# Kernel optimization log

Hardware: AMD Instinct MI355X
Metric: run time of the kernel (lower is better)

Reference implementation:

```python
import jax, jax.numpy as jnp
import numpy as np

NUM_SCOPE = 64
NUM_SAMPLE = 16
DIM_ENCODE = 64


def _fixed_basis(dim):
    # FixedTimeEncoder / FixedFrequencyEncoder basis: w_i = 1 / 10^(9*i/(dim-1))
    return (1.0 / 10.0 ** jnp.linspace(0.0, 9.0, dim)).astype(jnp.float32)


def _cos_encode(t, dim):
    # t: [...] -> [..., dim]
    w = _fixed_basis(dim)
    return jnp.cos(t[..., None] * w)


def setup_inputs() -> dict:
    key = jax.random.key(0)
    ks = jax.random.split(key, 12)
    n, b, df = 4096, NUM_SCOPE, 172
    s_in = 1.0 / np.sqrt(df)
    return {
        "root_node_feature": jax.random.normal(ks[0], (n, df), jnp.float32),
        "root_ts": jax.random.uniform(ks[1], (n,), jnp.float32) * 1e4,
        "neighbor_node_feature": jax.random.normal(ks[2], (n, b, df), jnp.float32),
        "neighbor_edge_feature": jax.random.normal(ks[3], (n, b, df), jnp.float32),
        "neighbor_ts": jax.random.uniform(ks[4], (n, b), jnp.float32) * 1e4,
        "neighbor_nid": jax.random.randint(ks[5], (n, b), 0, 10000, jnp.int64) if jax.config.jax_enable_x64 else jax.random.randint(ks[5], (n, b), 0, 10000, jnp.int32),
        "W_node": jax.random.normal(ks[6], (df, 64), jnp.float32) * s_in,
        "b_node": jnp.zeros((64,), jnp.float32),
        "W_edge": jax.random.normal(ks[7], (df, 64), jnp.float32) * s_in,
        "b_edge": jnp.zeros((64,), jnp.float32),
        "W_link": jax.random.normal(ks[8], (320, 256), jnp.float32) / np.sqrt(320),
        "W_root": jax.random.normal(ks[9], (192, 256), jnp.float32) / np.sqrt(192),
    }


def reference(root_node_feature, root_ts, neighbor_node_feature,
              neighbor_edge_feature, neighbor_ts, neighbor_nid,
              W_node, b_node, W_edge, b_edge, W_link, W_root):
    n, b = neighbor_nid.shape
    # --- encode root node ---
    root_feat = jax.nn.relu(root_node_feature @ W_node + b_node)          # [n,64]
    root_time = _cos_encode(jnp.zeros((n,), jnp.float32), DIM_ENCODE)     # [n,64]
    root_freq = _cos_encode(jnp.ones((n,), jnp.float32), DIM_ENCODE)      # [n,64]
    root_encode = jnp.concatenate([root_feat, root_time, root_freq], 1)   # [n,192]
    # --- encode links ---
    node_enc = jax.nn.relu(neighbor_node_feature @ W_node + b_node)       # [n,b,64]
    edge_enc = jax.nn.relu(neighbor_edge_feature @ W_edge + b_edge)       # [n,b,64]
    neigh_time = root_ts[:, None] - neighbor_ts                           # [n,b]
    time_enc = _cos_encode(neigh_time, DIM_ENCODE)                        # [n,b,64]
    # pairwise equality mask + frequency count (keep_dummy_freq=True)
    neigh_mask = (neighbor_nid[:, :, None] == neighbor_nid[:, None, :])   # [n,b,b]
    neigh_freq = neigh_mask.sum(-1).astype(jnp.float32) / NUM_SCOPE       # [n,b]
    freq_enc = _cos_encode(neigh_freq, DIM_ENCODE)                        # [n,b,64]
    iden_enc = neigh_mask.astype(jnp.float32)                             # [n,b,b]
    link_encode = jnp.concatenate(
        [node_enc, edge_enc, time_enc, freq_enc, iden_enc], axis=-1)      # [n,b,320]
    # --- link mapper: project links & root, score, softmax over neighbors ---
    h_link = jax.nn.relu(jnp.einsum('nbd,dh->nbh', link_encode, W_link))  # [n,b,256]
    h_root = jax.nn.relu(root_encode @ W_root)                            # [n,256]
    scores = jnp.einsum('nbh,nh->nb', h_link, h_root) / jnp.sqrt(256.0)
    probs = jax.nn.softmax(scores, axis=-1)                               # [n,b]
    # --- weighted sampling WITHOUT replacement via Gumbel top-k ---
    g = jax.random.gumbel(jax.random.key(42), (n, b), jnp.float32)
    logp = jnp.log(probs + 1e-20)
    _, action = jax.lax.top_k(logp + g, NUM_SAMPLE)                       # [n,num_sample]
    return probs, action
```

## Files before the change

### kernel.cpp

```cpp
#include <hip/hip_runtime.h>
#include <cstdint>
#include <math.h>

#define B       64
#define DF      172
#define HDIM    256
#define KSAMP   16
#define THREADS 512

typedef const __attribute__((address_space(1))) unsigned int* gp_t;
typedef __attribute__((address_space(3))) unsigned int* lp_t;

#define FMA4(A_, S_, W_) \
  A_.x = fmaf(S_, W_.x, A_.x); A_.y = fmaf(S_, W_.y, A_.y); \
  A_.z = fmaf(S_, W_.z, A_.z); A_.w = fmaf(S_, W_.w, A_.w);

__device__ __forceinline__ uint32_t rotl32(uint32_t x, int d) {
  return (x << d) | (x >> (32 - d));
}

__device__ __forceinline__ void threefry2x32(uint32_t k0, uint32_t k1,
                                             uint32_t& x0, uint32_t& x1) {
  const uint32_t ks0 = k0, ks1 = k1, ks2 = k0 ^ k1 ^ 0x1BD11BDAu;
  x0 += ks0; x1 += ks1;
#define TF_R4(ra,rb,rc,rd) \
  x0 += x1; x1 = rotl32(x1, ra); x1 ^= x0; \
  x0 += x1; x1 = rotl32(x1, rb); x1 ^= x0; \
  x0 += x1; x1 = rotl32(x1, rc); x1 ^= x0; \
  x0 += x1; x1 = rotl32(x1, rd); x1 ^= x0;
  TF_R4(13,15,26,6)  x0 += ks1; x1 += ks2 + 1u;
  TF_R4(17,29,16,24) x0 += ks2; x1 += ks0 + 2u;
  TF_R4(13,15,26,6)  x0 += ks0; x1 += ks1 + 3u;
  TF_R4(17,29,16,24) x0 += ks1; x1 += ks2 + 4u;
  TF_R4(13,15,26,6)  x0 += ks2; x1 += ks0 + 5u;
#undef TF_R4
}

__device__ __forceinline__ void stage_async(const float* __restrict__ g,
                                            float* l, int t) {
#pragma unroll
  for (int it = 0; it < 5; ++it) {
    const int i  = it * 512 + t;
    const int ib = it * 512 + (t & ~63);
    __builtin_amdgcn_global_load_lds((gp_t)(g + i * 4), (lp_t)(l + ib * 4), 16, 0, 0);
  }
  if (t < 192) {
    const int i  = 2560 + t;
    const int ib = 2560 + (t & ~63);
    __builtin_amdgcn_global_load_lds((gp_t)(g + i * 4), (lp_t)(l + ib * 4), 16, 0, 0);
  }
}

__device__ __forceinline__ void enc_gemm(const float* __restrict__ stage,
                                         const float* __restrict__ W,
                                         const float* __restrict__ bias,
                                         float* __restrict__ out,
                                         int b2, int cg) {
  const float4* W4 = (const float4*)W;
  const float4* A0 = (const float4*)(stage + (2 * b2) * DF);
  const float4* A1 = (const float4*)(stage + (2 * b2 + 1) * DF);
  float4 acc0 = ((const float4*)bias)[cg];
  float4 acc1 = acc0;
  float4 w0 = W4[0 * 16 + cg], w1 = W4[1 * 16 + cg];
  float4 w2 = W4[2 * 16 + cg], w3 = W4[3 * 16 + cg];
  for (int k = 0; k < DF; k += 4) {
    const float4 wa = w0, wb = w1, wc = w2, wd = w3;
    if (k < DF - 4) {
      w0 = W4[(k + 4) * 16 + cg]; w1 = W4[(k + 5) * 16 + cg];
      w2 = W4[(k + 6) * 16 + cg]; w3 = W4[(k + 7) * 16 + cg];
    }
    const float4 x0 = A0[k >> 2];
    const float4 x1 = A1[k >> 2];
    FMA4(acc0, x0.x, wa) FMA4(acc0, x0.y, wb) FMA4(acc0, x0.z, wc) FMA4(acc0, x0.w, wd)
    FMA4(acc1, x1.x, wa) FMA4(acc1, x1.y, wb) FMA4(acc1, x1.z, wc) FMA4(acc1, x1.w, wd)
  }
  float4 o0 = make_float4(fmaxf(acc0.x, 0.f), fmaxf(acc0.y, 0.f), fmaxf(acc0.z, 0.f), fmaxf(acc0.w, 0.f));
  float4 o1 = make_float4(fmaxf(acc1.x, 0.f), fmaxf(acc1.y, 0.f), fmaxf(acc1.z, 0.f), fmaxf(acc1.w, 0.f));
  ((float4*)out)[(2 * b2) * 16 + cg]     = o0;
  ((float4*)out)[(2 * b2 + 1) * 16 + cg] = o1;
}

__device__ __forceinline__ void accum16(float2 (&acc)[16],
                                        const float* __restrict__ enc, int r16,
                                        const float2* __restrict__ Wlp) {
  float2 w0 = Wlp[0], w1 = Wlp[128], w2 = Wlp[256], w3 = Wlp[384];
  for (int d0 = 0; d0 < 64; d0 += 4) {
    const float2 wa = w0, wb = w1, wc = w2, wd = w3;
    if (d0 < 60) {
      const float2* p = Wlp + (d0 + 4) * 128;
      w0 = p[0]; w1 = p[128]; w2 = p[256]; w3 = p[384];
    }
#pragma unroll
    for (int i = 0; i < 16; ++i) {
      const float4 e = *(const float4*)&enc[(r16 + i) * 64 + d0];
      acc[i].x = fmaf(e.x, wa.x, acc[i].x); acc[i].y = fmaf(e.x, wa.y, acc[i].y);
      acc[i].x = fmaf(e.y, wb.x, acc[i].x); acc[i].y = fmaf(e.y, wb.y, acc[i].y);
      acc[i].x = fmaf(e.z, wc.x, acc[i].x); acc[i].y = fmaf(e.z, wc.y, acc[i].y);
      acc[i].x = fmaf(e.w, wd.x, acc[i].x); acc[i].y = fmaf(e.w, wd.y, acc[i].y);
    }
  }
}

__global__ __launch_bounds__(THREADS, 4)
void AdaptSampler_kernel(const float* __restrict__ rootf,
                         const float* __restrict__ root_ts,
                         const float* __restrict__ nf,
                         const float* __restrict__ ef,
                         const float* __restrict__ nts,
                         const int*   __restrict__ nid,
                         const float* __restrict__ Wn,
                         const float* __restrict__ bn,
                         const float* __restrict__ We,
                         const float* __restrict__ be,
                         const float* __restrict__ Wl,
                         const float* __restrict__ Wr,
                         float* __restrict__ out_probs,
                         float* __restrict__ out_action)
{
  __shared__ float nf_stage[B * DF];
  __shared__ float encA[B * 64];
  __shared__ float encB[B * 64];
  __shared__ float hroot_lds[HDIM];
  __shared__ float rootenc_lds[192];
  __shared__ float w_lds[B];
  __shared__ float ts_lds[B];
  __shared__ __align__(16) int nid_lds[B];
  __shared__ float freq_lds[B];
  __shared__ unsigned long long mask_lds[B];
  __shared__ float scpart[4][16][2];

  const int n = blockIdx.x;
  const int t = threadIdx.x;
  const int c2  = t & 127;
  const int r16 = (t >> 7) * 16;
  const int b2 = t >> 4;
  const int cg = t & 15;
  const float2* Wl2 = (const float2*)Wl;

  stage_async(nf + (size_t)n * B * DF, nf_stage, t);
  if (t >= 448) {
    const int j = t - 448;
    double e = 9.0 * (double)j / 63.0;
    const float wj = (float)(1.0 / pow(10.0, e));
    w_lds[j]   = wj;
    nid_lds[j] = nid[n * B + j];
    ts_lds[j]  = nts[n * B + j];
    float a = bn[j];
    const float* rr = rootf + (size_t)n * DF;
#pragma unroll 4
    for (int d = 0; d < DF; ++d) a = fmaf(rr[d], Wn[d * 64 + j], a);
    rootenc_lds[j]       = fmaxf(a, 0.0f);
    rootenc_lds[64 + j]  = 1.0f;
    rootenc_lds[128 + j] = cosf(wj);
  }
  __syncthreads();

  enc_gemm(nf_stage, Wn, bn, encA, b2, cg);
  {
    const float rts = root_ts[n];
#pragma unroll
    for (int q = 0; q < 8; ++q) {
      const int idx = q * 512 + t;
      const int bb = idx >> 6, dd = idx & 63;
      encB[idx] = cosf((rts - ts_lds[bb]) * w_lds[dd]);
    }
  }
  {
    const int h = t >> 1, hf = t & 1;
    float a = 0.0f;
    for (int d = hf * 96; d < hf * 96 + 96; ++d)
      a = fmaf(rootenc_lds[d], Wr[d * HDIM + h], a);
    a += __shfl_xor(a, 1);
    if (hf == 0) hroot_lds[h] = fmaxf(a, 0.0f);
  }
  if (t >= 448) {
    const int j = t - 448;
    const int my = nid_lds[j];
    unsigned long long m = 0ull;
    for (int k = 0; k < B; ++k)
      m |= ((unsigned long long)(nid_lds[k] == my)) << k;
    mask_lds[j] = m;
    freq_lds[j] = (float)__popcll(m) * 0.015625f;
  }
  __syncthreads();

  stage_async(ef + (size_t)n * B * DF, nf_stage, t);
  float2 acc[16];
#pragma unroll
  for (int i = 0; i < 16; ++i) acc[i] = make_float2(0.f, 0.f);
  accum16(acc, encA, r16, Wl2 + c2);
  __syncthreads();

  enc_gemm(nf_stage, We, be, encA, b2, cg);
  __syncthreads();

  accum16(acc, encA, r16, Wl2 + 64 * 128 + c2);
  __syncthreads();

#pragma unroll
  for (int q = 0; q < 8; ++q) {
    const int idx = q * 512 + t;
    const int bb = idx >> 6, dd = idx & 63;
    encA[idx] = cosf(freq_lds[bb] * w_lds[dd]);
  }
  __syncthreads();

  accum16(acc, encB, r16, Wl2 + 128 * 128 + c2);
  accum16(acc, encA, r16, Wl2 + 192 * 128 + c2);
  {
    const float2* Wlp = Wl2 + 256 * 128 + c2;
#pragma unroll
    for (int i = 0; i < 16; ++i) {
      unsigned long long m = mask_lds[r16 + i];
      while (m) {
        const int d = __builtin_ctzll(m);
        m &= m - 1;
        const float2 wv = Wlp[d * 128];
        acc[i].x += wv.x;
        acc[i].y += wv.y;
      }
    }
  }

  {
    const float2 hr = ((const float2*)hroot_lds)[c2];
#pragma unroll
    for (int i = 0; i < 16; ++i) {
      float s = fmaxf(acc[i].x, 0.f) * hr.x;
      s = fmaf(fmaxf(acc[i].y, 0.f), hr.y, s);
#pragma unroll
      for (int mm = 32; mm >= 1; mm >>= 1) s += __shfl_xor(s, mm);
      if ((t & 63) == 0) scpart[t >> 7][i][(t >> 6) & 1] = s;
    }
  }
  __syncthreads();

  if (t < B) {
    float s = (scpart[t >> 4][t & 15][0] + scpart[t >> 4][t & 15][1]) * 0.0625f;
    float m = s;
#pragma unroll
    for (int mm = 32; mm >= 1; mm >>= 1) m = fmaxf(m, __shfl_xor(m, mm));
    float e = expf(s - m);
    float sum = e;
#pragma unroll
    for (int mm = 32; mm >= 1; mm >>= 1) sum += __shfl_xor(sum, mm);
    float p = e / sum;
    out_probs[(size_t)n * B + t] = p;

    uint32_t i = (uint32_t)(n * B + t);
    uint32_t x0 = 0u, x1 = i;
    threefry2x32(0u, 42u, x0, x1);
    uint32_t bits = x0 ^ x1;
    float f = __uint_as_float((bits >> 9) | 0x3f800000u) - 1.0f;
    const float TINY = 1.1754943508222875e-38f;
    float u = fmaxf(f * (1.0f - TINY) + TINY, TINY);
    float g = -logf(-logf(u));
    float keyv = logf(p + 1e-20f) + g;

    float v = keyv;
    for (int k = 0; k < KSAMP; ++k) {
      float bv = v; int bi = t;
#pragma unroll
      for (int mm = 32; mm >= 1; mm >>= 1) {
        float ov = __shfl_xor(bv, mm);
        int   oi = __shfl_xor(bi, mm);
        if (ov > bv || (ov == bv && oi < bi)) { bv = ov; bi = oi; }
      }
      if (t == 0) out_action[(size_t)n * KSAMP + k] = (float)bi;
      if (t == bi) v = -3.402823466e+38f;
    }
  }
}

extern "C" void kernel_launch(void* const* d_in, const int* in_sizes, int n_in,
                              void* d_out, int out_size, void* d_ws, size_t ws_size,
                              hipStream_t stream) {
  const float* rootf = (const float*)d_in[0];
  const float* rts   = (const float*)d_in[1];
  const float* nf    = (const float*)d_in[2];
  const float* ef    = (const float*)d_in[3];
  const float* nts   = (const float*)d_in[4];
  const int*   nid   = (const int*)d_in[5];
  const float* Wn    = (const float*)d_in[6];
  const float* bn    = (const float*)d_in[7];
  const float* We    = (const float*)d_in[8];
  const float* be    = (const float*)d_in[9];
  const float* Wl    = (const float*)d_in[10];
  const float* Wr    = (const float*)d_in[11];

  const int n = in_sizes[1];
  float* probs  = (float*)d_out;
  float* action = probs + (size_t)n * B;

  AdaptSampler_kernel<<<dim3(n), dim3(THREADS), 0, stream>>>(
      rootf, rts, nf, ef, nts, nid, Wn, bn, We, be, Wl, Wr, probs, action);
}
```

Measured before the change: 882.4 us.

## Deepen weight prefetch in enc_gemm, move mask build earlier, drop one barrier

The encoder GEMM loop now keeps three groups of weight loads in flight with a manual 3-stage rotation instead of one-step lookahead. The neighbor-id mask and frequency computation moves into the first setup block. The frequency cosine encoding is written into the free staging buffer so it can overlap with the edge-encoding accumulation, removing one __syncthreads. This adds register pressure from the extra float4 prefetch registers and reuses the staging buffer, which has to be free by then.

```diff
diff --git a/kernel.cpp b/kernel.cpp
--- a/kernel.cpp
+++ b/kernel.cpp
@@ -51,6 +51,16 @@
   }
 }
 
+#define ENC_STEP(W0_, W1_, W2_, W3_, KK_) { \
+  const float4 x0 = A0[(KK_) >> 2]; \
+  const float4 x1 = A1[(KK_) >> 2]; \
+  FMA4(acc0, x0.x, W0_) FMA4(acc0, x0.y, W1_) FMA4(acc0, x0.z, W2_) FMA4(acc0, x0.w, W3_) \
+  FMA4(acc1, x1.x, W0_) FMA4(acc1, x1.y, W1_) FMA4(acc1, x1.z, W2_) FMA4(acc1, x1.w, W3_) }
+
+#define ENC_LOAD(W0_, W1_, W2_, W3_, KK_) { \
+  W0_ = W4[(KK_) * 16 + cg]; W1_ = W4[((KK_) + 1) * 16 + cg]; \
+  W2_ = W4[((KK_) + 2) * 16 + cg]; W3_ = W4[((KK_) + 3) * 16 + cg]; }
+
 __device__ __forceinline__ void enc_gemm(const float* __restrict__ stage,
                                          const float* __restrict__ W,
                                          const float* __restrict__ bias,
@@ -61,19 +71,19 @@
   const float4* A1 = (const float4*)(stage + (2 * b2 + 1) * DF);
   float4 acc0 = ((const float4*)bias)[cg];
   float4 acc1 = acc0;
-  float4 w0 = W4[0 * 16 + cg], w1 = W4[1 * 16 + cg];
-  float4 w2 = W4[2 * 16 + cg], w3 = W4[3 * 16 + cg];
-  for (int k = 0; k < DF; k += 4) {
-    const float4 wa = w0, wb = w1, wc = w2, wd = w3;
-    if (k < DF - 4) {
-      w0 = W4[(k + 4) * 16 + cg]; w1 = W4[(k + 5) * 16 + cg];
-      w2 = W4[(k + 6) * 16 + cg]; w3 = W4[(k + 7) * 16 + cg];
-    }
-    const float4 x0 = A0[k >> 2];
-    const float4 x1 = A1[k >> 2];
-    FMA4(acc0, x0.x, wa) FMA4(acc0, x0.y, wb) FMA4(acc0, x0.z, wc) FMA4(acc0, x0.w, wd)
-    FMA4(acc1, x1.x, wa) FMA4(acc1, x1.y, wb) FMA4(acc1, x1.z, wc) FMA4(acc1, x1.w, wd)
-  }
+  float4 a0, a1, a2, a3, b0, b1, b2_, b3, c0, c1, c2, c3;
+  ENC_LOAD(a0, a1, a2, a3, 0)
+  ENC_LOAD(b0, b1, b2_, b3, 4)
+  ENC_LOAD(c0, c1, c2, c3, 8)
+  for (int k0 = 0; k0 < 156; k0 += 12) {
+    ENC_STEP(a0, a1, a2, a3, k0)       ENC_LOAD(a0, a1, a2, a3, k0 + 12)
+    ENC_STEP(b0, b1, b2_, b3, k0 + 4)  ENC_LOAD(b0, b1, b2_, b3, k0 + 16)
+    ENC_STEP(c0, c1, c2, c3, k0 + 8)   ENC_LOAD(c0, c1, c2, c3, k0 + 20)
+  }
+  ENC_STEP(a0, a1, a2, a3, 156)  ENC_LOAD(a0, a1, a2, a3, 168)
+  ENC_STEP(b0, b1, b2_, b3, 160)
+  ENC_STEP(c0, c1, c2, c3, 164)
+  ENC_STEP(a0, a1, a2, a3, 168)
   float4 o0 = make_float4(fmaxf(acc0.x, 0.f), fmaxf(acc0.y, 0.f), fmaxf(acc0.z, 0.f), fmaxf(acc0.w, 0.f));
   float4 o1 = make_float4(fmaxf(acc1.x, 0.f), fmaxf(acc1.y, 0.f), fmaxf(acc1.z, 0.f), fmaxf(acc1.w, 0.f));
   ((float4*)out)[(2 * b2) * 16 + cg]     = o0;
@@ -152,6 +162,12 @@
     rootenc_lds[j]       = fmaxf(a, 0.0f);
     rootenc_lds[64 + j]  = 1.0f;
     rootenc_lds[128 + j] = cosf(wj);
+    const int my = nid_lds[j];
+    unsigned long long m = 0ull;
+    for (int k = 0; k < B; ++k)
+      m |= ((unsigned long long)(nid_lds[k] == my)) << k;
+    mask_lds[j] = m;
+    freq_lds[j] = (float)__popcll(m) * 0.015625f;
   }
   __syncthreads();
 
@@ -173,15 +189,6 @@
     a += __shfl_xor(a, 1);
     if (hf == 0) hroot_lds[h] = fmaxf(a, 0.0f);
   }
-  if (t >= 448) {
-    const int j = t - 448;
-    const int my = nid_lds[j];
-    unsigned long long m = 0ull;
-    for (int k = 0; k < B; ++k)
-      m |= ((unsigned long long)(nid_lds[k] == my)) << k;
-    mask_lds[j] = m;
-    freq_lds[j] = (float)__popcll(m) * 0.015625f;
-  }
   __syncthreads();
 
   stage_async(ef + (size_t)n * B * DF, nf_stage, t);
@@ -192,21 +199,19 @@
   __syncthreads();
 
   enc_gemm(nf_stage, We, be, encA, b2, cg);
-  __syncthreads();
-
-  accum16(acc, encA, r16, Wl2 + 64 * 128 + c2);
   __syncthreads();
 
 #pragma unroll
   for (int q = 0; q < 8; ++q) {
     const int idx = q * 512 + t;
     const int bb = idx >> 6, dd = idx & 63;
-    encA[idx] = cosf(freq_lds[bb] * w_lds[dd]);
-  }
+    nf_stage[idx] = cosf(freq_lds[bb] * w_lds[dd]);
+  }
+  accum16(acc, encA, r16, Wl2 + 64 * 128 + c2);
   __syncthreads();
 
   accum16(acc, encB, r16, Wl2 + 128 * 128 + c2);
-  accum16(acc, encA, r16, Wl2 + 192 * 128 + c2);
+  accum16(acc, nf_stage, r16, Wl2 + 192 * 128 + c2);
   {
     const float2* Wlp = Wl2 + 256 * 128 + c2;
 #pragma unroll
```

Result: slower. 966.2 us (+9.5%).

## Read encoder inputs directly from global and drop LDS staging buffer

Applied to the files above, without the earlier changes.

Removes the async global-to-LDS staging of neighbor node/edge features and has the encoder GEMM read rows straight from global memory with software prefetch. Both encoder GEMMs now run back to back into separate LDS buffers, the mask computation moves earlier, and several barriers disappear. The freed LDS and a higher launch-bounds occupancy hint aim to fit more blocks per CU. It risks uncoalesced strided global reads and register spilling under the tighter register budget.

```diff
diff --git a/kernel.cpp b/kernel.cpp
--- a/kernel.cpp
+++ b/kernel.cpp
@@ -7,9 +7,6 @@
 #define HDIM    256
 #define KSAMP   16
 #define THREADS 512
-
-typedef const __attribute__((address_space(1))) unsigned int* gp_t;
-typedef __attribute__((address_space(3))) unsigned int* lp_t;
 
 #define FMA4(A_, S_, W_) \
   A_.x = fmaf(S_, W_.x, A_.x); A_.y = fmaf(S_, W_.y, A_.y); \
@@ -36,43 +33,32 @@
 #undef TF_R4
 }
 
-__device__ __forceinline__ void stage_async(const float* __restrict__ g,
-                                            float* l, int t) {
-#pragma unroll
-  for (int it = 0; it < 5; ++it) {
-    const int i  = it * 512 + t;
-    const int ib = it * 512 + (t & ~63);
-    __builtin_amdgcn_global_load_lds((gp_t)(g + i * 4), (lp_t)(l + ib * 4), 16, 0, 0);
-  }
-  if (t < 192) {
-    const int i  = 2560 + t;
-    const int ib = 2560 + (t & ~63);
-    __builtin_amdgcn_global_load_lds((gp_t)(g + i * 4), (lp_t)(l + ib * 4), 16, 0, 0);
-  }
-}
-
-__device__ __forceinline__ void enc_gemm(const float* __restrict__ stage,
-                                         const float* __restrict__ W,
-                                         const float* __restrict__ bias,
-                                         float* __restrict__ out,
-                                         int b2, int cg) {
+#define ENC_FMA(W0_, W1_, W2_, W3_, X0_, X1_) { \
+  FMA4(acc0, X0_.x, W0_) FMA4(acc0, X0_.y, W1_) FMA4(acc0, X0_.z, W2_) FMA4(acc0, X0_.w, W3_) \
+  FMA4(acc1, X1_.x, W0_) FMA4(acc1, X1_.y, W1_) FMA4(acc1, X1_.z, W2_) FMA4(acc1, X1_.w, W3_) }
+
+__device__ __forceinline__ void enc_gemm_g(const float* __restrict__ gA,
+                                           const float* __restrict__ W,
+                                           const float* __restrict__ bias,
+                                           float* __restrict__ out,
+                                           int b2, int cg) {
   const float4* W4 = (const float4*)W;
-  const float4* A0 = (const float4*)(stage + (2 * b2) * DF);
-  const float4* A1 = (const float4*)(stage + (2 * b2 + 1) * DF);
+  const float4* A0 = (const float4*)(gA + (size_t)(2 * b2) * DF);
+  const float4* A1 = (const float4*)(gA + (size_t)(2 * b2 + 1) * DF);
   float4 acc0 = ((const float4*)bias)[cg];
   float4 acc1 = acc0;
   float4 w0 = W4[0 * 16 + cg], w1 = W4[1 * 16 + cg];
   float4 w2 = W4[2 * 16 + cg], w3 = W4[3 * 16 + cg];
+  float4 x0 = A0[0], x1 = A1[0];
   for (int k = 0; k < DF; k += 4) {
     const float4 wa = w0, wb = w1, wc = w2, wd = w3;
+    const float4 xa = x0, xb = x1;
     if (k < DF - 4) {
       w0 = W4[(k + 4) * 16 + cg]; w1 = W4[(k + 5) * 16 + cg];
       w2 = W4[(k + 6) * 16 + cg]; w3 = W4[(k + 7) * 16 + cg];
-    }
-    const float4 x0 = A0[k >> 2];
-    const float4 x1 = A1[k >> 2];
-    FMA4(acc0, x0.x, wa) FMA4(acc0, x0.y, wb) FMA4(acc0, x0.z, wc) FMA4(acc0, x0.w, wd)
-    FMA4(acc1, x1.x, wa) FMA4(acc1, x1.y, wb) FMA4(acc1, x1.z, wc) FMA4(acc1, x1.w, wd)
+      x0 = A0[(k >> 2) + 1];      x1 = A1[(k >> 2) + 1];
+    }
+    ENC_FMA(wa, wb, wc, wd, xa, xb)
   }
   float4 o0 = make_float4(fmaxf(acc0.x, 0.f), fmaxf(acc0.y, 0.f), fmaxf(acc0.z, 0.f), fmaxf(acc0.w, 0.f));
   float4 o1 = make_float4(fmaxf(acc1.x, 0.f), fmaxf(acc1.y, 0.f), fmaxf(acc1.z, 0.f), fmaxf(acc1.w, 0.f));
@@ -101,7 +87,7 @@
   }
 }
 
-__global__ __launch_bounds__(THREADS, 4)
+__global__ __launch_bounds__(THREADS, 6)
 void AdaptSampler_kernel(const float* __restrict__ rootf,
                          const float* __restrict__ root_ts,
                          const float* __restrict__ nf,
@@ -117,9 +103,9 @@
                          float* __restrict__ out_probs,
                          float* __restrict__ out_action)
 {
-  __shared__ float nf_stage[B * DF];
   __shared__ float encA[B * 64];
   __shared__ float encB[B * 64];
+  __shared__ float encC[B * 64];
   __shared__ float hroot_lds[HDIM];
   __shared__ float rootenc_lds[192];
   __shared__ float w_lds[B];
@@ -137,7 +123,6 @@
   const int cg = t & 15;
   const float2* Wl2 = (const float2*)Wl;
 
-  stage_async(nf + (size_t)n * B * DF, nf_stage, t);
   if (t >= 448) {
     const int j = t - 448;
     double e = 9.0 * (double)j / 63.0;
@@ -152,10 +137,17 @@
     rootenc_lds[j]       = fmaxf(a, 0.0f);
     rootenc_lds[64 + j]  = 1.0f;
     rootenc_lds[128 + j] = cosf(wj);
-  }
-  __syncthreads();
-
-  enc_gemm(nf_stage, Wn, bn, encA, b2, cg);
+    const int my = nid_lds[j];
+    unsigned long long m = 0ull;
+    for (int k = 0; k < B; ++k)
+      m |= ((unsigned long long)(nid_lds[k] == my)) << k;
+    mask_lds[j] = m;
+    freq_lds[j] = (float)__popcll(m) * 0.015625f;
+  }
+  __syncthreads();
+
+  enc_gemm_g(nf + (size_t)n * B * DF, Wn, bn, encA, b2, cg);
+  enc_gemm_g(ef + (size_t)n * B * DF, We, be, encC, b2, cg);
   {
     const float rts = root_ts[n];
 #pragma unroll
@@ -173,40 +165,25 @@
     a += __shfl_xor(a, 1);
     if (hf == 0) hroot_lds[h] = fmaxf(a, 0.0f);
   }
-  if (t >= 448) {
-    const int j = t - 448;
-    const int my = nid_lds[j];
-    unsigned long long m = 0ull;
-    for (int k = 0; k < B; ++k)
-      m |= ((unsigned long long)(nid_lds[k] == my)) << k;
-    mask_lds[j] = m;
-    freq_lds[j] = (float)__popcll(m) * 0.015625f;
-  }
-  __syncthreads();
-
-  stage_async(ef + (size_t)n * B * DF, nf_stage, t);
+  __syncthreads();
+
   float2 acc[16];
 #pragma unroll
   for (int i = 0; i < 16; ++i) acc[i] = make_float2(0.f, 0.f);
   accum16(acc, encA, r16, Wl2 + c2);
-  __syncthreads();
-
-  enc_gemm(nf_stage, We, be, encA, b2, cg);
-  __syncthreads();
-
-  accum16(acc, encA, r16, Wl2 + 64 * 128 + c2);
+  accum16(acc, encC, r16, Wl2 + 64 * 128 + c2);
+  accum16(acc, encB, r16, Wl2 + 128 * 128 + c2);
   __syncthreads();
 
 #pragma unroll
   for (int q = 0; q < 8; ++q) {
     const int idx = q * 512 + t;
     const int bb = idx >> 6, dd = idx & 63;
-    encA[idx] = cosf(freq_lds[bb] * w_lds[dd]);
-  }
-  __syncthreads();
-
-  accum16(acc, encB, r16, Wl2 + 128 * 128 + c2);
-  accum16(acc, encA, r16, Wl2 + 192 * 128 + c2);
+    encB[idx] = cosf(freq_lds[bb] * w_lds[dd]);
+  }
+  __syncthreads();
+
+  accum16(acc, encB, r16, Wl2 + 192 * 128 + c2);
   {
     const float2* Wlp = Wl2 + 256 * 128 + c2;
 #pragma unroll
@@ -221,7 +198,6 @@
       }
     }
   }
-
   {
     const float2 hr = ((const float2*)hroot_lds)[c2];
 #pragma unroll
```

New measurement: 1.023 ms. 15.9% more time.
